# Optimization experiments

Hardware: AMD Instinct MI355X
Metric: run time of the kernel (lower is better)

Reference implementation:

```python
import jax, jax.numpy as jnp
import numpy as np

EPS = 1e-7
INF = 1e8
NUM_CLASSES = 80
SOFT_CENTER_RADIUS = 3.0
TOPK = 13
IOU_WEIGHT = 3.0

B, N, G, C = 16, 8400, 100, NUM_CLASSES
IMG = 640.0


def setup_inputs() -> dict:
    key = jax.random.key(0)
    ks = jax.random.split(key, 8)
    # anchor priors: centers in image, stride column (cx, cy, s, s)
    ctr = jax.random.uniform(ks[0], (N, 2)) * IMG
    stride = jnp.full((N, 1), 8.0)
    priors = jnp.concatenate([ctr, stride, stride], axis=-1)
    # predicted boxes: xyxy around random centers
    pc = jax.random.uniform(ks[1], (B, N, 2)) * IMG
    pwh = jax.random.uniform(ks[2], (B, N, 2)) * 64.0 + 8.0
    pred_bboxes = jnp.concatenate([pc - pwh / 2, pc + pwh / 2], axis=-1)
    pred_scores = jax.random.normal(ks[3], (B, N, C))
    # gt boxes: xyxy
    gc = jax.random.uniform(ks[4], (B, G, 2)) * (IMG - 40.0) + 20.0
    gwh = jax.random.uniform(ks[5], (B, G, 2)) * 128.0 + 16.0
    gt_bboxes = jnp.concatenate([gc - gwh / 2, gc + gwh / 2], axis=-1)
    gt_labels = jax.random.randint(ks[6], (B, G, 1), 0, NUM_CLASSES, dtype=jnp.int32)
    pad_bbox_flag = jnp.ones((B, G, 1), dtype=jnp.float32)
    gt_bboxes_area = gwh[..., 0] * gwh[..., 1]
    area_rule = jnp.array([0.0, 32.0, 96.0, 1.0e4], dtype=jnp.float32)
    return {
        'pred_bboxes': pred_bboxes, 'pred_scores': pred_scores, 'priors': priors,
        'gt_labels': gt_labels, 'gt_bboxes': gt_bboxes, 'pad_bbox_flag': pad_bbox_flag,
        'gt_bboxes_area': gt_bboxes_area, 'area_rule': area_rule,
    }


def _giou(b1, b2):
    # b1, b2 broadcastable [..., 4] xyxy -> GIoU [...]
    lt = jnp.maximum(b1[..., :2], b2[..., :2])
    rb = jnp.minimum(b1[..., 2:], b2[..., 2:])
    wh = jnp.clip(rb - lt, 0.0)
    overlap = wh[..., 0] * wh[..., 1]
    a1 = (b1[..., 2] - b1[..., 0]) * (b1[..., 3] - b1[..., 1])
    a2 = (b2[..., 2] - b2[..., 0]) * (b2[..., 3] - b2[..., 1])
    union = jnp.maximum(a1 + a2 - overlap, EPS)
    iou = overlap / union
    elt = jnp.minimum(b1[..., :2], b2[..., :2])
    erb = jnp.maximum(b1[..., 2:], b2[..., 2:])
    ewh = jnp.clip(erb - elt, 0.0)
    enclose = jnp.maximum(ewh[..., 0] * ewh[..., 1], EPS)
    return iou - (enclose - union) / enclose


def _forward(pred_bboxes, pred_scores, priors, gt_labels, gt_bboxes, pad_bbox_flag,
             gt_bboxes_area, area_rule):
    b, n, _ = pred_bboxes.shape
    g = gt_bboxes.shape[1]
    pts = priors[:, :2]                      # (N,2)
    # point-in-box test -> (B,N,G)
    lt = pts[None, :, None, :] - gt_bboxes[:, None, :, :2]
    rb = gt_bboxes[:, None, :, 2:] - pts[None, :, None, :]
    deltas = jnp.concatenate([lt, rb], axis=-1)          # (B,N,G,4)
    is_in = (jnp.min(deltas, axis=-1) > 0).astype(pred_bboxes.dtype)
    is_in = is_in * pad_bbox_flag[:, None, :, 0]
    # soft center prior
    gt_ctr = (gt_bboxes[..., :2] + gt_bboxes[..., 2:]) / 2.0
    strides = priors[:, 2]
    dist = jnp.sqrt(((pts[None, :, None, :] - gt_ctr[:, None, :, :]) ** 2).sum(-1))
    dist = dist / strides[None, :, None] * is_in
    soft_center_prior = jnp.power(10.0, dist - SOFT_CENTER_RADIUS) * is_in
    # pairwise GIoU (B,N,G)
    giou = _giou(pred_bboxes[:, :, None, :], gt_bboxes[:, None, :, :])
    pairwise_ious = jnp.abs(giou * is_in)
    iou_cost = -jnp.log(pairwise_ious + EPS) * IOU_WEIGHT
    # per-gt-class logit gather: (B,N,G)
    labels = gt_labels[..., 0].astype(jnp.int32)         # (B,G)
    idx = jnp.broadcast_to(labels[:, None, :], (b, n, g))
    logits = jnp.take_along_axis(pred_scores, idx, axis=2)
    sig = jax.nn.sigmoid(logits)
    scale = pairwise_ious - sig
    # stable BCE-with-logits against soft target pairwise_ious
    bce = jnp.maximum(logits, 0.0) - logits * pairwise_ious + jnp.log1p(jnp.exp(-jnp.abs(logits)))
    cls_cost = bce * jnp.exp(jnp.abs(scale) - 1.0) * jnp.abs(scale)
    cost = cls_cost + iou_cost + soft_center_prior
    in_mask = is_in > 0
    cost = jnp.where(in_mask, cost, INF)
    # dynamic-k matching
    k = min(TOPK, n)
    topk_ious = jax.lax.top_k(jnp.transpose(pairwise_ious, (0, 2, 1)), k)[0]  # (B,G,k)
    dyn_k = jnp.clip(topk_ious.sum(-1).astype(jnp.int32), 1, None)            # (B,G)
    ranks = jnp.argsort(jnp.argsort(cost, axis=1), axis=1)                    # (B,N,G)
    valid_gt = pad_bbox_flag[..., 0] > 0                                      # (B,G)
    matching = (ranks < dyn_k[:, None, :]) & valid_gt[:, None, :]             # (B,N,G)
    # resolve anchors matched to >1 gt: keep min-cost gt
    multi = matching.sum(-1) > 1                                              # (B,N)
    onehot_min = jax.nn.one_hot(jnp.argmin(cost, axis=-1), g, dtype=jnp.bool_)
    matching = jnp.where(multi[..., None], onehot_min, matching)
    fg_mask = matching.sum(-1) > 0                                            # (B,N)
    mf = matching.astype(pairwise_ious.dtype)
    matched_ious = (mf * pairwise_ious).sum(-1)                               # (B,N)
    matched_gt = jnp.argmax(mf, axis=-1)                                      # (B,N)
    # dense assignments
    assigned_labels = jnp.where(fg_mask, jnp.take_along_axis(labels, matched_gt, axis=1), NUM_CLASSES)
    gidx = jnp.broadcast_to(matched_gt[..., None], (b, n, 4))
    assigned_bboxes = jnp.where(fg_mask[..., None], jnp.take_along_axis(gt_bboxes, gidx, axis=1), 0.0)
    assign_metrics = jnp.where(fg_mask, matched_ious, 0.0)
    onehot = jax.nn.one_hot(assigned_labels, NUM_CLASSES + 1, dtype=pred_scores.dtype)[..., :NUM_CLASSES]
    assigned_scores = onehot * jnp.where(fg_mask, matched_ious, 1.0)[..., None]
    # per-class positive counts and dynamic class weights
    assigned_labels_num = (onehot * fg_mask[..., None].astype(onehot.dtype)).sum((0, 1))
    maxc = assigned_labels_num.max()
    dynamic_gt_class_weight = jnp.where(assigned_labels_num > 0,
                                        maxc / jnp.maximum(assigned_labels_num, 1.0), 1.0)
    assigned_labels_weights = jnp.where(fg_mask[..., None],
                                        dynamic_gt_class_weight[None, None, :],
                                        jnp.ones((), pred_scores.dtype))
    # gt area distribution (len(area_rule)-1, B, G)
    r2 = area_rule ** 2
    ga = gt_bboxes_area[None]
    area_dist = (ga >= r2[:-1, None, None]) & (ga < r2[1:, None, None]) & valid_gt[None]
    return (assigned_labels.astype(jnp.int32), assigned_labels_weights, assigned_bboxes,
            assigned_scores, assign_metrics, fg_mask, assigned_labels_num,
            dynamic_gt_class_weight, area_dist)


def reference(pred_bboxes, pred_scores, priors, gt_labels, gt_bboxes, pad_bbox_flag,
              gt_bboxes_area, area_rule):
    return _forward(pred_bboxes, pred_scores, priors, gt_labels, gt_bboxes,
                    pad_bbox_flag, gt_bboxes_area, area_rule)
```

## Files before the change

### kernel.cpp

```cpp
#include <hip/hip_runtime.h>

typedef unsigned long long u64;

#define BB 16
#define NN 8400
#define GG 100
#define CC 80
#define KTOP 13
#define EPSF 1e-7f
#define INFC 1e8f
#define MAXIN 1024
#define MAXMULTI (BB * GG * KTOP / 2)

static constexpr size_t kO_LAB  = 0;
static constexpr size_t kO_W    = (size_t)BB * NN;
static constexpr size_t kO_BB   = kO_W + (size_t)BB * NN * CC;
static constexpr size_t kO_SC   = kO_BB + (size_t)BB * NN * 4;
static constexpr size_t kO_MET  = kO_SC + (size_t)BB * NN * CC;
static constexpr size_t kO_FG   = kO_MET + (size_t)BB * NN;
static constexpr size_t kO_NUM  = kO_FG + (size_t)BB * NN;
static constexpr size_t kO_DYNW = kO_NUM + CC;
static constexpr size_t kO_AREA = kO_DYNW + CC;

__device__ __forceinline__ unsigned f2u(float x) {
    unsigned b = __float_as_uint(x);
    return (b & 0x80000000u) ? ~b : (b | 0x80000000u);
}
__device__ __forceinline__ float u2f(unsigned e) {
    return __uint_as_float((e & 0x80000000u) ? (e & 0x7fffffffu) : ~e);
}

__device__ __forceinline__ void pair_cost_iou_inside(
    float px, float py, float st,
    float p0, float p1, float p2, float p3,
    float g0, float g1, float g2, float g3,
    float lg, float flag,
    float& cost, float& piou)
{
    float gcx = (g0 + g2) * 0.5f, gcy = (g1 + g3) * 0.5f;
    float dx = px - gcx, dy = py - gcy;
    float dist = sqrtf(dx * dx + dy * dy) / st * flag;
    float scp = exp2f((dist - 3.0f) * 3.32192809488736f) * flag;
    float ix1 = fmaxf(p0, g0), iy1 = fmaxf(p1, g1);
    float ix2 = fminf(p2, g2), iy2 = fminf(p3, g3);
    float ow = fmaxf(ix2 - ix1, 0.0f), oh = fmaxf(iy2 - iy1, 0.0f);
    float ov = ow * oh;
    float a1 = (p2 - p0) * (p3 - p1);
    float a2 = (g2 - g0) * (g3 - g1);
    float uni = fmaxf(a1 + a2 - ov, EPSF);
    float iou = ov / uni;
    float ex1 = fminf(p0, g0), ey1 = fminf(p1, g1);
    float ex2 = fmaxf(p2, g2), ey2 = fmaxf(p3, g3);
    float ew = fmaxf(ex2 - ex1, 0.0f), eh = fmaxf(ey2 - ey1, 0.0f);
    float enc = fmaxf(ew * eh, EPSF);
    float giou = iou - (enc - uni) / enc;
    piou = fabsf(giou * flag);
    float iou_cost = -__logf(piou + EPSF) * 3.0f;
    float sig = 1.0f / (1.0f + __expf(-lg));
    float sc = piou - sig;
    float asc = fabsf(sc);
    float bce = fmaxf(lg, 0.0f) - lg * piou + log1pf(__expf(-fabsf(lg)));
    float cls = bce * __expf(asc - 1.0f) * asc;
    cost = cls + iou_cost + scp;
}

__device__ __forceinline__ void pair_cost_iou(
    float px, float py, float st,
    float p0, float p1, float p2, float p3,
    float g0, float g1, float g2, float g3,
    float lg, float flag,
    float& cost, float& piou)
{
    float l = px - g0, t = py - g1, r = g2 - px, d = g3 - py;
    float mn = fminf(fminf(l, t), fminf(r, d));
    float is_in = (mn > 0.0f) ? flag : 0.0f;
    float gcx = (g0 + g2) * 0.5f, gcy = (g1 + g3) * 0.5f;
    float dx = px - gcx, dy = py - gcy;
    float dist = sqrtf(dx * dx + dy * dy) / st * is_in;
    float scp = exp2f((dist - 3.0f) * 3.32192809488736f) * is_in;
    float ix1 = fmaxf(p0, g0), iy1 = fmaxf(p1, g1);
    float ix2 = fminf(p2, g2), iy2 = fminf(p3, g3);
    float ow = fmaxf(ix2 - ix1, 0.0f), oh = fmaxf(iy2 - iy1, 0.0f);
    float ov = ow * oh;
    float a1 = (p2 - p0) * (p3 - p1);
    float a2 = (g2 - g0) * (g3 - g1);
    float uni = fmaxf(a1 + a2 - ov, EPSF);
    float iou = ov / uni;
    float ex1 = fminf(p0, g0), ey1 = fminf(p1, g1);
    float ex2 = fmaxf(p2, g2), ey2 = fmaxf(p3, g3);
    float ew = fmaxf(ex2 - ex1, 0.0f), eh = fmaxf(ey2 - ey1, 0.0f);
    float enc = fmaxf(ew * eh, EPSF);
    float giou = iou - (enc - uni) / enc;
    piou = fabsf(giou * is_in);
    float iou_cost = -__logf(piou + EPSF) * 3.0f;
    float sig = 1.0f / (1.0f + __expf(-lg));
    float sc = piou - sig;
    float asc = fabsf(sc);
    float bce = fmaxf(lg, 0.0f) - lg * piou + log1pf(__expf(-fabsf(lg)));
    float cls = bce * __expf(asc - 1.0f) * asc;
    float cc = cls + iou_cost + scp;
    cost = (is_in > 0.0f) ? cc : INFC;
}

__device__ __forceinline__ u64 block_max_u64(u64 v, u64* s_red, int tid) {
    #pragma unroll
    for (int off = 32; off > 0; off >>= 1) {
        u64 o = __shfl_down(v, off, 64);
        if (o > v) v = o;
    }
    __syncthreads();
    if ((tid & 63) == 0) s_red[tid >> 6] = v;
    __syncthreads();
    u64 m = s_red[0];
    #pragma unroll
    for (int i = 1; i < 4; ++i) if (s_red[i] > m) m = s_red[i];
    return m;
}
__device__ __forceinline__ u64 block_min_u64(u64 v, u64* s_red, int tid) {
    #pragma unroll
    for (int off = 32; off > 0; off >>= 1) {
        u64 o = __shfl_down(v, off, 64);
        if (o < v) v = o;
    }
    __syncthreads();
    if ((tid & 63) == 0) s_red[tid >> 6] = v;
    __syncthreads();
    u64 m = s_red[0];
    #pragma unroll
    for (int i = 1; i < 4; ++i) if (s_red[i] < m) m = s_red[i];
    return m;
}

__global__ __launch_bounds__(256) void k1_match(
    const float* __restrict__ pred_bboxes,
    const float* __restrict__ pred_scores,
    const float* __restrict__ priors,
    const int*   __restrict__ gt_labels,
    const float* __restrict__ gt_bboxes,
    const float* __restrict__ pad_flag,
    int*   __restrict__ match_count,
    int*   __restrict__ match_g,
    float* __restrict__ match_iou)
{
    __shared__ int s_cnt;
    __shared__ int s_list[MAXIN];
    __shared__ u64 s_red[4];

    int bg = blockIdx.x;
    int b = bg / GG, g = bg - b * GG;
    int tid = threadIdx.x;

    float flag = pad_flag[bg];
    if (flag == 0.0f) return;

    if (tid == 0) s_cnt = 0;
    __syncthreads();

    float4 gb = *reinterpret_cast<const float4*>(gt_bboxes + (size_t)bg * 4);

    for (int n = tid; n < NN; n += 256) {
        float2 p = *reinterpret_cast<const float2*>(priors + (size_t)n * 4);
        float l = p.x - gb.x, t = p.y - gb.y;
        float r = gb.z - p.x, d = gb.w - p.y;
        float mn = fminf(fminf(l, t), fminf(r, d));
        if (mn > 0.0f) {
            int po = atomicAdd(&s_cnt, 1);
            if (po < MAXIN) s_list[po] = n;
        }
    }
    __syncthreads();
    int M = min(s_cnt, MAXIN);

    if (M == 0) {
        if (tid == 0) {
            int idx = b * NN;
            atomicAdd(&match_count[idx], 1);
            match_g[idx]   = g;
            match_iou[idx] = 0.0f;
        }
        return;
    }

    int lab = gt_labels[bg];

    u64 zs = ((u64)0x80000000u << 32) | (0x10000u + (unsigned)tid * 4u);
    u64 iK0 = zs, iK1 = zs + 1, iK2 = zs + 2, iK3 = zs + 3;
    u64 cK0 = ~0ull, cK1 = ~0ull, cK2 = ~0ull, cK3 = ~0ull;
    float cP0 = 0.f, cP1 = 0.f, cP2 = 0.f, cP3 = 0.f;

    for (int m = tid; m < M; m += 256) {
        int n = s_list[m];
        float4 pr = *reinterpret_cast<const float4*>(priors + (size_t)n * 4);
        float4 pb = *reinterpret_cast<const float4*>(pred_bboxes + ((size_t)b * NN + n) * 4);
        float lg = pred_scores[((size_t)b * NN + n) * CC + lab];
        float cost, piou;
        pair_cost_iou_inside(pr.x, pr.y, pr.z, pb.x, pb.y, pb.z, pb.w,
                             gb.x, gb.y, gb.z, gb.w, lg, flag, cost, piou);
        u64 ki = ((u64)f2u(piou) << 32) | (unsigned)n;
        if (ki > iK3) {
            iK3 = ki;
            if (iK3 > iK2) { u64 t0 = iK2; iK2 = iK3; iK3 = t0; }
            if (iK2 > iK1) { u64 t0 = iK1; iK1 = iK2; iK2 = t0; }
            if (iK1 > iK0) { u64 t0 = iK0; iK0 = iK1; iK1 = t0; }
        }
        u64 kc = ((u64)f2u(cost) << 32) | (unsigned)n;
        if (kc < cK3) {
            cK3 = kc; cP3 = piou;
            if (cK3 < cK2) { u64 t0 = cK2; cK2 = cK3; cK3 = t0; float f0 = cP2; cP2 = cP3; cP3 = f0; }
            if (cK2 < cK1) { u64 t0 = cK1; cK1 = cK2; cK2 = t0; float f0 = cP1; cP1 = cP2; cP2 = f0; }
            if (cK1 < cK0) { u64 t0 = cK0; cK0 = cK1; cK1 = t0; float f0 = cP0; cP0 = cP1; cP1 = f0; }
        }
    }

    float ksum = 0.0f;
    for (int it = 0; it < KTOP; ++it) {
        u64 mx = block_max_u64(iK0, s_red, tid);
        ksum += u2f((unsigned)(mx >> 32));
        if (iK0 == mx) { iK0 = iK1; iK1 = iK2; iK2 = iK3; iK3 = 0ull; }
    }
    int dyn_k = (int)ksum;
    if (dyn_k < 1) dyn_k = 1;

    for (int it = 0; it < dyn_k; ++it) {
        u64 mn = block_min_u64(cK0, s_red, tid);
        if (cK0 == mn) {
            int bi = (int)(mn & 0xffffffffu);
            int idx = b * NN + bi;
            atomicAdd(&match_count[idx], 1);
            match_g[idx]   = g;
            match_iou[idx] = cP0;
            cK0 = cK1; cP0 = cP1; cK1 = cK2; cP1 = cP2; cK2 = cK3; cP2 = cP3;
            cK3 = ~0ull;
        }
    }
}

__global__ __launch_bounds__(256) void k2a_resolve(
    const int*   __restrict__ gt_labels,
    const float* __restrict__ gt_bboxes,
    const int*   __restrict__ match_count,
    const int*   __restrict__ match_g,
    const float* __restrict__ match_iou,
    int*   __restrict__ r_lab,
    float* __restrict__ r_miou,
    int*   __restrict__ class_num,
    int*   __restrict__ multi_count,
    int*   __restrict__ multi_list,
    float* __restrict__ out)
{
    int i = blockIdx.x * 256 + threadIdx.x;
    if (i >= BB * NN) return;
    int cnt = match_count[i];
    if (cnt > 1) {
        int p = atomicAdd(multi_count, 1);
        multi_list[p] = i;
        return;
    }
    int b = i / NN;
    int lab = CC;
    float miou = 0.0f;
    float4 bb = make_float4(0.0f, 0.0f, 0.0f, 0.0f);
    if (cnt == 1) {
        int g = match_g[i];
        miou = match_iou[i];
        lab = gt_labels[b * GG + g];
        bb = *reinterpret_cast<const float4*>(gt_bboxes + (size_t)(b * GG + g) * 4);
        atomicAdd(&class_num[lab], 1);
    }
    r_lab[i]  = lab;
    r_miou[i] = miou;
    out[kO_LAB + i] = (float)lab;
    out[kO_FG  + i] = (cnt == 1) ? 1.0f : 0.0f;
    out[kO_MET + i] = miou;
    *reinterpret_cast<float4*>(out + kO_BB + (size_t)i * 4) = bb;
}

__global__ __launch_bounds__(256) void k2b_multi(
    const float* __restrict__ pred_bboxes,
    const float* __restrict__ pred_scores,
    const float* __restrict__ priors,
    const int*   __restrict__ gt_labels,
    const float* __restrict__ gt_bboxes,
    const float* __restrict__ pad_flag,
    const int*   __restrict__ multi_count,
    const int*   __restrict__ multi_list,
    int*   __restrict__ r_lab,
    float* __restrict__ r_miou,
    int*   __restrict__ class_num,
    float* __restrict__ out)
{
    int wid  = (blockIdx.x * 256 + threadIdx.x) >> 6;
    int lane = threadIdx.x & 63;
    int cnt = *multi_count;
    if (wid >= cnt) return;
    int i = multi_list[wid];
    int b = i / NN, n = i - b * NN;

    float4 pr = *reinterpret_cast<const float4*>(priors + (size_t)n * 4);
    float4 pb = *reinterpret_cast<const float4*>(pred_bboxes + (size_t)i * 4);

    u64 bestk = ~0ull;
    float bestiou = 0.0f;
    #pragma unroll
    for (int s = 0; s < 2; ++s) {
        int g = lane + s * 64;
        if (g < GG) {
            float flag = pad_flag[b * GG + g];
            float4 gb = *reinterpret_cast<const float4*>(gt_bboxes + (size_t)(b * GG + g) * 4);
            int lb = gt_labels[b * GG + g];
            float lg = pred_scores[(size_t)i * CC + lb];
            float cost, piou;
            pair_cost_iou(pr.x, pr.y, pr.z, pb.x, pb.y, pb.z, pb.w,
                          gb.x, gb.y, gb.z, gb.w, lg, flag, cost, piou);
            u64 k = ((u64)f2u(cost) << 32) | (unsigned)g;
            if (k < bestk) { bestk = k; bestiou = piou; }
        }
    }
    #pragma unroll
    for (int off = 32; off > 0; off >>= 1) {
        u64 ok = __shfl_down(bestk, off, 64);
        float op = __shfl_down(bestiou, off, 64);
        if (ok < bestk) { bestk = ok; bestiou = op; }
    }
    if (lane == 0) {
        int g = (int)(bestk & 0xffffffffu);
        int lab = gt_labels[b * GG + g];
        float4 bb = *reinterpret_cast<const float4*>(gt_bboxes + (size_t)(b * GG + g) * 4);
        atomicAdd(&class_num[lab], 1);
        r_lab[i]  = lab;
        r_miou[i] = bestiou;
        out[kO_LAB + i] = (float)lab;
        out[kO_FG  + i] = 1.0f;
        out[kO_MET + i] = bestiou;
        *reinterpret_cast<float4*>(out + kO_BB + (size_t)i * 4) = bb;
    }
}

__global__ void k3_weights(const int* __restrict__ class_num,
                           float* __restrict__ dynw,
                           float* __restrict__ out)
{
    int lane = threadIdx.x;
    int n0 = class_num[lane];
    int n1 = (lane < CC - 64) ? class_num[lane + 64] : 0;
    int m = max(n0, n1);
    #pragma unroll
    for (int off = 32; off > 0; off >>= 1) m = max(m, __shfl_down(m, off, 64));
    m = __shfl(m, 0, 64);
    float fm = (float)m;
    {
        float w = (n0 > 0) ? fm / fmaxf((float)n0, 1.0f) : 1.0f;
        dynw[lane] = w;
        out[kO_NUM  + lane] = (float)n0;
        out[kO_DYNW + lane] = w;
    }
    if (lane < CC - 64) {
        float w = (n1 > 0) ? fm / fmaxf((float)n1, 1.0f) : 1.0f;
        dynw[lane + 64] = w;
        out[kO_NUM  + lane + 64] = (float)n1;
        out[kO_DYNW + lane + 64] = w;
    }
}

__global__ __launch_bounds__(256) void k4_fill(
    const int*   __restrict__ r_lab,
    const float* __restrict__ r_miou,
    const float* __restrict__ dynw,
    float* __restrict__ out)
{
    __shared__ float s_w[CC];
    if (threadIdx.x < CC) s_w[threadIdx.x] = dynw[threadIdx.x];
    __syncthreads();
    unsigned t = blockIdx.x * 256u + threadIdx.x;
    unsigned i = t / 20u;
    unsigned cq = (t - i * 20u) * 4u;
    int lab = r_lab[i];
    float miou = r_miou[i];
    bool fg = lab < CC;
    unsigned ulab = (unsigned)lab;
    float4 sc, wv;
    sc.x = (ulab == cq + 0u) ? miou : 0.0f;
    sc.y = (ulab == cq + 1u) ? miou : 0.0f;
    sc.z = (ulab == cq + 2u) ? miou : 0.0f;
    sc.w = (ulab == cq + 3u) ? miou : 0.0f;
    wv.x = fg ? s_w[cq + 0u] : 1.0f;
    wv.y = fg ? s_w[cq + 1u] : 1.0f;
    wv.z = fg ? s_w[cq + 2u] : 1.0f;
    wv.w = fg ? s_w[cq + 3u] : 1.0f;
    size_t base = (size_t)i * CC + cq;
    *reinterpret_cast<float4*>(out + kO_SC + base) = sc;
    *reinterpret_cast<float4*>(out + kO_W  + base) = wv;
}

__global__ void k5_area(const float* __restrict__ gt_area,
                        const float* __restrict__ area_rule,
                        const float* __restrict__ pad_flag,
                        float* __restrict__ out)
{
    int idx = blockIdx.x * 256 + threadIdx.x;
    if (idx >= 3 * BB * GG) return;
    int z = idx / (BB * GG);
    int rem = idx - z * (BB * GG);
    float ga = gt_area[rem];
    float lo = area_rule[z] * area_rule[z];
    float hi = area_rule[z + 1] * area_rule[z + 1];
    bool v = (ga >= lo) && (ga < hi) && (pad_flag[rem] > 0.0f);
    out[kO_AREA + idx] = v ? 1.0f : 0.0f;
}

extern "C" void kernel_launch(void* const* d_in, const int* in_sizes, int n_in,
                              void* d_out, int out_size, void* d_ws, size_t ws_size,
                              hipStream_t stream)
{
    const float* pred_bboxes = (const float*)d_in[0];
    const float* pred_scores = (const float*)d_in[1];
    const float* priors      = (const float*)d_in[2];
    const int*   gt_labels   = (const int*)d_in[3];
    const float* gt_bboxes   = (const float*)d_in[4];
    const float* pad_flag    = (const float*)d_in[5];
    const float* gt_area     = (const float*)d_in[6];
    const float* area_rule   = (const float*)d_in[7];
    float* out = (float*)d_out;

    char* w = (char*)d_ws;
    int*   match_count = (int*)w;   w += (size_t)BB * NN * 4;
    int*   class_num   = (int*)w;   w += (size_t)CC * 4;
    int*   multi_count = (int*)w;   w += 4;
    int*   multi_list  = (int*)w;   w += (size_t)MAXMULTI * 4;
    int*   match_g     = (int*)w;   w += (size_t)BB * NN * 4;
    float* match_iou   = (float*)w; w += (size_t)BB * NN * 4;
    int*   r_lab       = (int*)w;   w += (size_t)BB * NN * 4;
    float* r_miou      = (float*)w; w += (size_t)BB * NN * 4;
    float* dynw        = (float*)w; w += (size_t)CC * 4;

    hipMemsetAsync(d_ws, 0, (size_t)(BB * NN + CC + 1) * 4, stream);

    k1_match<<<BB * GG, 256, 0, stream>>>(
        pred_bboxes, pred_scores, priors, gt_labels, gt_bboxes, pad_flag,
        match_count, match_g, match_iou);

    k2a_resolve<<<(BB * NN + 255) / 256, 256, 0, stream>>>(
        gt_labels, gt_bboxes, match_count, match_g, match_iou,
        r_lab, r_miou, class_num, multi_count, multi_list, out);

    k2b_multi<<<(MAXMULTI * 64 + 255) / 256, 256, 0, stream>>>(
        pred_bboxes, pred_scores, priors, gt_labels, gt_bboxes, pad_flag,
        multi_count, multi_list, r_lab, r_miou, class_num, out);

    k3_weights<<<1, 64, 0, stream>>>(class_num, dynw, out);

    k4_fill<<<(int)(((size_t)BB * NN * (CC / 4) + 255) / 256), 256, 0, stream>>>(
        r_lab, r_miou, dynw, out);

    k5_area<<<(3 * BB * GG + 255) / 256, 256, 0, stream>>>(
        gt_area, area_rule, pad_flag, out);
}
```

Baseline: 240.1 us.

## Replace block-wide top-k reductions with per-wave selection and merge kernels

The top-k IoU and dynamic-k cost selections in the match kernel now run per wave with xor shuffles, and a single wave merges the candidates. This replaces a block reduction with two barriers per iteration. The separate multi-match resolve kernel is folded into the resolve kernel through a ballot loop, the weights and area kernels are merged, and the prior scan is unrolled. The result is fewer launches and barriers, at the cost of divergent per-wave loops inside the resolve kernel.

```diff
diff --git a/kernel.cpp b/kernel.cpp
--- a/kernel.cpp
+++ b/kernel.cpp
@@ -10,7 +10,6 @@
 #define EPSF 1e-7f
 #define INFC 1e8f
 #define MAXIN 1024
-#define MAXMULTI (BB * GG * KTOP / 2)
 
 static constexpr size_t kO_LAB  = 0;
 static constexpr size_t kO_W    = (size_t)BB * NN;
@@ -102,35 +101,6 @@
     cost = (is_in > 0.0f) ? cc : INFC;
 }
 
-__device__ __forceinline__ u64 block_max_u64(u64 v, u64* s_red, int tid) {
-    #pragma unroll
-    for (int off = 32; off > 0; off >>= 1) {
-        u64 o = __shfl_down(v, off, 64);
-        if (o > v) v = o;
-    }
-    __syncthreads();
-    if ((tid & 63) == 0) s_red[tid >> 6] = v;
-    __syncthreads();
-    u64 m = s_red[0];
-    #pragma unroll
-    for (int i = 1; i < 4; ++i) if (s_red[i] > m) m = s_red[i];
-    return m;
-}
-__device__ __forceinline__ u64 block_min_u64(u64 v, u64* s_red, int tid) {
-    #pragma unroll
-    for (int off = 32; off > 0; off >>= 1) {
-        u64 o = __shfl_down(v, off, 64);
-        if (o < v) v = o;
-    }
-    __syncthreads();
-    if ((tid & 63) == 0) s_red[tid >> 6] = v;
-    __syncthreads();
-    u64 m = s_red[0];
-    #pragma unroll
-    for (int i = 1; i < 4; ++i) if (s_red[i] < m) m = s_red[i];
-    return m;
-}
-
 __global__ __launch_bounds__(256) void k1_match(
     const float* __restrict__ pred_bboxes,
     const float* __restrict__ pred_scores,
@@ -142,13 +112,17 @@
     int*   __restrict__ match_g,
     float* __restrict__ match_iou)
 {
-    __shared__ int s_cnt;
-    __shared__ int s_list[MAXIN];
-    __shared__ u64 s_red[4];
+    __shared__ int   s_cnt;
+    __shared__ int   s_list[MAXIN];
+    __shared__ u64   s_cand[4 * KTOP];
+    __shared__ float s_candP[4 * KTOP];
+    __shared__ int   s_dynk;
 
     int bg = blockIdx.x;
     int b = bg / GG, g = bg - b * GG;
-    int tid = threadIdx.x;
+    int tid  = threadIdx.x;
+    int lane = tid & 63;
+    int w    = tid >> 6;
 
     float flag = pad_flag[bg];
     if (flag == 0.0f) return;
@@ -158,11 +132,22 @@
 
     float4 gb = *reinterpret_cast<const float4*>(gt_bboxes + (size_t)bg * 4);
 
-    for (int n = tid; n < NN; n += 256) {
-        float2 p = *reinterpret_cast<const float2*>(priors + (size_t)n * 4);
-        float l = p.x - gb.x, t = p.y - gb.y;
-        float r = gb.z - p.x, d = gb.w - p.y;
-        float mn = fminf(fminf(l, t), fminf(r, d));
+    #pragma unroll 4
+    for (int k = 0; k < 32; ++k) {
+        int n = tid + (k << 8);
+        float4 p = *reinterpret_cast<const float4*>(priors + (size_t)n * 4);
+        float mn = fminf(fminf(p.x - gb.x, p.y - gb.y),
+                         fminf(gb.z - p.x, gb.w - p.y));
+        if (mn > 0.0f) {
+            int po = atomicAdd(&s_cnt, 1);
+            if (po < MAXIN) s_list[po] = n;
+        }
+    }
+    if (tid < NN - 8192) {
+        int n = tid + 8192;
+        float4 p = *reinterpret_cast<const float4*>(priors + (size_t)n * 4);
+        float mn = fminf(fminf(p.x - gb.x, p.y - gb.y),
+                         fminf(gb.z - p.x, gb.w - p.y));
         if (mn > 0.0f) {
             int po = atomicAdd(&s_cnt, 1);
             if (po < MAXIN) s_list[po] = n;
@@ -212,153 +197,202 @@
         }
     }
 
-    float ksum = 0.0f;
-    for (int it = 0; it < KTOP; ++it) {
-        u64 mx = block_max_u64(iK0, s_red, tid);
-        ksum += u2f((unsigned)(mx >> 32));
-        if (iK0 == mx) { iK0 = iK1; iK1 = iK2; iK2 = iK3; iK3 = 0ull; }
-    }
-    int dyn_k = (int)ksum;
-    if (dyn_k < 1) dyn_k = 1;
-
-    for (int it = 0; it < dyn_k; ++it) {
-        u64 mn = block_min_u64(cK0, s_red, tid);
-        if (cK0 == mn) {
-            int bi = (int)(mn & 0xffffffffu);
-            int idx = b * NN + bi;
-            atomicAdd(&match_count[idx], 1);
-            match_g[idx]   = g;
-            match_iou[idx] = cP0;
+    for (int r = 0; r < KTOP; ++r) {
+        u64 h = iK0;
+        #pragma unroll
+        for (int off = 1; off < 64; off <<= 1) {
+            u64 o = __shfl_xor(h, off, 64);
+            if (o > h) h = o;
+        }
+        if (lane == 0) s_cand[w * KTOP + r] = h;
+        if (iK0 == h) { iK0 = iK1; iK1 = iK2; iK2 = iK3; iK3 = 0ull; }
+    }
+    __syncthreads();
+    if (w == 0) {
+        u64 kk = (lane < 4 * KTOP) ? s_cand[lane] : 0ull;
+        float ks = 0.0f;
+        for (int r = 0; r < KTOP; ++r) {
+            u64 h = kk;
+            #pragma unroll
+            for (int off = 1; off < 64; off <<= 1) {
+                u64 o = __shfl_xor(h, off, 64);
+                if (o > h) h = o;
+            }
+            ks += u2f((unsigned)(h >> 32));
+            if (kk == h) kk = 0ull;
+        }
+        if (lane == 0) { int dk = (int)ks; s_dynk = (dk < 1) ? 1 : dk; }
+    }
+    __syncthreads();
+    int dyn_k = s_dynk;
+
+    for (int r = 0; r < dyn_k; ++r) {
+        u64 h = cK0;
+        #pragma unroll
+        for (int off = 1; off < 64; off <<= 1) {
+            u64 o = __shfl_xor(h, off, 64);
+            if (o < h) h = o;
+        }
+        if (cK0 == h) {
+            s_cand[w * KTOP + r]  = h;
+            s_candP[w * KTOP + r] = cP0;
             cK0 = cK1; cP0 = cP1; cK1 = cK2; cP1 = cP2; cK2 = cK3; cP2 = cP3;
             cK3 = ~0ull;
         }
     }
-}
-
-__global__ __launch_bounds__(256) void k2a_resolve(
+    __syncthreads();
+    if (w == 0) {
+        int tot = 4 * dyn_k;
+        u64 kk = ~0ull; float pp = 0.0f;
+        if (lane < tot) {
+            int wv = lane / dyn_k;
+            int r  = lane - wv * dyn_k;
+            kk = s_cand[wv * KTOP + r];
+            pp = s_candP[wv * KTOP + r];
+        }
+        for (int r = 0; r < dyn_k; ++r) {
+            u64 h = kk;
+            #pragma unroll
+            for (int off = 1; off < 64; off <<= 1) {
+                u64 o = __shfl_xor(h, off, 64);
+                if (o < h) h = o;
+            }
+            if (kk == h && h != ~0ull) {
+                int bi = (int)(h & 0xffffffffu);
+                int idx = b * NN + bi;
+                atomicAdd(&match_count[idx], 1);
+                match_g[idx]   = g;
+                match_iou[idx] = pp;
+                kk = ~0ull;
+            }
+        }
+    }
+}
+
+__global__ __launch_bounds__(256) void k2_resolve(
+    const float* __restrict__ pred_bboxes,
+    const float* __restrict__ pred_scores,
+    const float* __restrict__ priors,
     const int*   __restrict__ gt_labels,
     const float* __restrict__ gt_bboxes,
+    const float* __restrict__ pad_flag,
     const int*   __restrict__ match_count,
     const int*   __restrict__ match_g,
     const float* __restrict__ match_iou,
     int*   __restrict__ r_lab,
     float* __restrict__ r_miou,
     int*   __restrict__ class_num,
-    int*   __restrict__ multi_count,
-    int*   __restrict__ multi_list,
     float* __restrict__ out)
 {
     int i = blockIdx.x * 256 + threadIdx.x;
-    if (i >= BB * NN) return;
+    int lane = threadIdx.x & 63;
     int cnt = match_count[i];
-    if (cnt > 1) {
-        int p = atomicAdd(multi_count, 1);
-        multi_list[p] = i;
-        return;
-    }
     int b = i / NN;
+
     int lab = CC;
     float miou = 0.0f;
-    float4 bb = make_float4(0.0f, 0.0f, 0.0f, 0.0f);
+    float4 bbx = make_float4(0.0f, 0.0f, 0.0f, 0.0f);
+
     if (cnt == 1) {
         int g = match_g[i];
+        int gi = b * GG + g;
         miou = match_iou[i];
-        lab = gt_labels[b * GG + g];
-        bb = *reinterpret_cast<const float4*>(gt_bboxes + (size_t)(b * GG + g) * 4);
-        atomicAdd(&class_num[lab], 1);
-    }
+        lab = gt_labels[gi];
+        bbx = *reinterpret_cast<const float4*>(gt_bboxes + (size_t)gi * 4);
+    }
+
+    u64 mask = __ballot(cnt > 1);
+    while (mask) {
+        int src = __builtin_ctzll(mask);
+        mask &= mask - 1;
+        int ii = (i & ~63) | src;
+        int b2 = ii / NN, n2 = ii - b2 * NN;
+        float4 pr = *reinterpret_cast<const float4*>(priors + (size_t)n2 * 4);
+        float4 pb = *reinterpret_cast<const float4*>(pred_bboxes + (size_t)ii * 4);
+        u64 bk = ~0ull; float bp = 0.0f;
+        #pragma unroll
+        for (int s = 0; s < 2; ++s) {
+            int gg = lane + (s << 6);
+            if (gg < GG) {
+                int gi = b2 * GG + gg;
+                float fl = pad_flag[gi];
+                float4 gbx = *reinterpret_cast<const float4*>(gt_bboxes + (size_t)gi * 4);
+                int lb = gt_labels[gi];
+                float lg = pred_scores[(size_t)ii * CC + lb];
+                float cost, piou;
+                pair_cost_iou(pr.x, pr.y, pr.z, pb.x, pb.y, pb.z, pb.w,
+                              gbx.x, gbx.y, gbx.z, gbx.w, lg, fl, cost, piou);
+                u64 k = ((u64)f2u(cost) << 32) | (unsigned)gg;
+                if (k < bk) { bk = k; bp = piou; }
+            }
+        }
+        #pragma unroll
+        for (int off = 1; off < 64; off <<= 1) {
+            u64 ok = __shfl_xor(bk, off, 64);
+            float op = __shfl_xor(bp, off, 64);
+            if (ok < bk) { bk = ok; bp = op; }
+        }
+        if (lane == src) {
+            int gw = (int)(bk & 0xffffffffu);
+            int gi = b2 * GG + gw;
+            lab = gt_labels[gi];
+            miou = bp;
+            bbx = *reinterpret_cast<const float4*>(gt_bboxes + (size_t)gi * 4);
+        }
+    }
+
+    bool fg = cnt > 0;
+    if (fg) atomicAdd(&class_num[lab], 1);
     r_lab[i]  = lab;
     r_miou[i] = miou;
     out[kO_LAB + i] = (float)lab;
-    out[kO_FG  + i] = (cnt == 1) ? 1.0f : 0.0f;
+    out[kO_FG  + i] = fg ? 1.0f : 0.0f;
     out[kO_MET + i] = miou;
-    *reinterpret_cast<float4*>(out + kO_BB + (size_t)i * 4) = bb;
-}
-
-__global__ __launch_bounds__(256) void k2b_multi(
-    const float* __restrict__ pred_bboxes,
-    const float* __restrict__ pred_scores,
-    const float* __restrict__ priors,
-    const int*   __restrict__ gt_labels,
-    const float* __restrict__ gt_bboxes,
+    *reinterpret_cast<float4*>(out + kO_BB + (size_t)i * 4) = bbx;
+}
+
+__global__ __launch_bounds__(256) void k35_weights_area(
+    const int*   __restrict__ class_num,
+    float* __restrict__ dynw,
+    const float* __restrict__ gt_area,
+    const float* __restrict__ area_rule,
     const float* __restrict__ pad_flag,
-    const int*   __restrict__ multi_count,
-    const int*   __restrict__ multi_list,
-    int*   __restrict__ r_lab,
-    float* __restrict__ r_miou,
-    int*   __restrict__ class_num,
     float* __restrict__ out)
 {
-    int wid  = (blockIdx.x * 256 + threadIdx.x) >> 6;
-    int lane = threadIdx.x & 63;
-    int cnt = *multi_count;
-    if (wid >= cnt) return;
-    int i = multi_list[wid];
-    int b = i / NN, n = i - b * NN;
-
-    float4 pr = *reinterpret_cast<const float4*>(priors + (size_t)n * 4);
-    float4 pb = *reinterpret_cast<const float4*>(pred_bboxes + (size_t)i * 4);
-
-    u64 bestk = ~0ull;
-    float bestiou = 0.0f;
-    #pragma unroll
-    for (int s = 0; s < 2; ++s) {
-        int g = lane + s * 64;
-        if (g < GG) {
-            float flag = pad_flag[b * GG + g];
-            float4 gb = *reinterpret_cast<const float4*>(gt_bboxes + (size_t)(b * GG + g) * 4);
-            int lb = gt_labels[b * GG + g];
-            float lg = pred_scores[(size_t)i * CC + lb];
-            float cost, piou;
-            pair_cost_iou(pr.x, pr.y, pr.z, pb.x, pb.y, pb.z, pb.w,
-                          gb.x, gb.y, gb.z, gb.w, lg, flag, cost, piou);
-            u64 k = ((u64)f2u(cost) << 32) | (unsigned)g;
-            if (k < bestk) { bestk = k; bestiou = piou; }
-        }
-    }
-    #pragma unroll
-    for (int off = 32; off > 0; off >>= 1) {
-        u64 ok = __shfl_down(bestk, off, 64);
-        float op = __shfl_down(bestiou, off, 64);
-        if (ok < bestk) { bestk = ok; bestiou = op; }
-    }
-    if (lane == 0) {
-        int g = (int)(bestk & 0xffffffffu);
-        int lab = gt_labels[b * GG + g];
-        float4 bb = *reinterpret_cast<const float4*>(gt_bboxes + (size_t)(b * GG + g) * 4);
-        atomicAdd(&class_num[lab], 1);
-        r_lab[i]  = lab;
-        r_miou[i] = bestiou;
-        out[kO_LAB + i] = (float)lab;
-        out[kO_FG  + i] = 1.0f;
-        out[kO_MET + i] = bestiou;
-        *reinterpret_cast<float4*>(out + kO_BB + (size_t)i * 4) = bb;
-    }
-}
-
-__global__ void k3_weights(const int* __restrict__ class_num,
-                           float* __restrict__ dynw,
-                           float* __restrict__ out)
-{
-    int lane = threadIdx.x;
-    int n0 = class_num[lane];
-    int n1 = (lane < CC - 64) ? class_num[lane + 64] : 0;
-    int m = max(n0, n1);
-    #pragma unroll
-    for (int off = 32; off > 0; off >>= 1) m = max(m, __shfl_down(m, off, 64));
-    m = __shfl(m, 0, 64);
-    float fm = (float)m;
-    {
-        float w = (n0 > 0) ? fm / fmaxf((float)n0, 1.0f) : 1.0f;
-        dynw[lane] = w;
-        out[kO_NUM  + lane] = (float)n0;
-        out[kO_DYNW + lane] = w;
-    }
-    if (lane < CC - 64) {
-        float w = (n1 > 0) ? fm / fmaxf((float)n1, 1.0f) : 1.0f;
-        dynw[lane + 64] = w;
-        out[kO_NUM  + lane + 64] = (float)n1;
-        out[kO_DYNW + lane + 64] = w;
+    if (blockIdx.x == 0) {
+        int lane = threadIdx.x;
+        if (lane < 64) {
+            int n0 = class_num[lane];
+            int n1 = (lane < CC - 64) ? class_num[lane + 64] : 0;
+            int m = max(n0, n1);
+            #pragma unroll
+            for (int off = 32; off > 0; off >>= 1) m = max(m, __shfl_down(m, off, 64));
+            m = __shfl(m, 0, 64);
+            float fm = (float)m;
+            {
+                float wv = (n0 > 0) ? fm / fmaxf((float)n0, 1.0f) : 1.0f;
+                dynw[lane] = wv;
+                out[kO_NUM  + lane] = (float)n0;
+                out[kO_DYNW + lane] = wv;
+            }
+            if (lane < CC - 64) {
+                float wv = (n1 > 0) ? fm / fmaxf((float)n1, 1.0f) : 1.0f;
+                dynw[lane + 64] = wv;
+                out[kO_NUM  + lane + 64] = (float)n1;
+                out[kO_DYNW + lane + 64] = wv;
+            }
+        }
+    } else {
+        int idx = (blockIdx.x - 1) * 256 + threadIdx.x;
+        if (idx < 3 * BB * GG) {
+            int z = idx / (BB * GG);
+            int rem = idx - z * (BB * GG);
+            float ga = gt_area[rem];
+            float lo = area_rule[z] * area_rule[z];
+            float hi = area_rule[z + 1] * area_rule[z + 1];
+            bool v = (ga >= lo) && (ga < hi) && (pad_flag[rem] > 0.0f);
+            out[kO_AREA + idx] = v ? 1.0f : 0.0f;
+        }
     }
 }
 
@@ -392,22 +426,6 @@
     *reinterpret_cast<float4*>(out + kO_W  + base) = wv;
 }
 
-__global__ void k5_area(const float* __restrict__ gt_area,
-                        const float* __restrict__ area_rule,
-                        const float* __restrict__ pad_flag,
-                        float* __restrict__ out)
-{
-    int idx = blockIdx.x * 256 + threadIdx.x;
-    if (idx >= 3 * BB * GG) return;
-    int z = idx / (BB * GG);
-    int rem = idx - z * (BB * GG);
-    float ga = gt_area[rem];
-    float lo = area_rule[z] * area_rule[z];
-    float hi = area_rule[z + 1] * area_rule[z + 1];
-    bool v = (ga >= lo) && (ga < hi) && (pad_flag[rem] > 0.0f);
-    out[kO_AREA + idx] = v ? 1.0f : 0.0f;
-}
-
 extern "C" void kernel_launch(void* const* d_in, const int* in_sizes, int n_in,
                               void* d_out, int out_size, void* d_ws, size_t ws_size,
                               hipStream_t stream)
@@ -425,33 +443,25 @@
     char* w = (char*)d_ws;
     int*   match_count = (int*)w;   w += (size_t)BB * NN * 4;
     int*   class_num   = (int*)w;   w += (size_t)CC * 4;
-    int*   multi_count = (int*)w;   w += 4;
-    int*   multi_list  = (int*)w;   w += (size_t)MAXMULTI * 4;
     int*   match_g     = (int*)w;   w += (size_t)BB * NN * 4;
     float* match_iou   = (float*)w; w += (size_t)BB * NN * 4;
     int*   r_lab       = (int*)w;   w += (size_t)BB * NN * 4;
     float* r_miou      = (float*)w; w += (size_t)BB * NN * 4;
     float* dynw        = (float*)w; w += (size_t)CC * 4;
 
-    hipMemsetAsync(d_ws, 0, (size_t)(BB * NN + CC + 1) * 4, stream);
+    hipMemsetAsync(d_ws, 0, (size_t)(BB * NN + CC) * 4, stream);
 
     k1_match<<<BB * GG, 256, 0, stream>>>(
         pred_bboxes, pred_scores, priors, gt_labels, gt_bboxes, pad_flag,
         match_count, match_g, match_iou);
 
-    k2a_resolve<<<(BB * NN + 255) / 256, 256, 0, stream>>>(
-        gt_labels, gt_bboxes, match_count, match_g, match_iou,
-        r_lab, r_miou, class_num, multi_count, multi_list, out);
-
-    k2b_multi<<<(MAXMULTI * 64 + 255) / 256, 256, 0, stream>>>(
+    k2_resolve<<<BB * NN / 256, 256, 0, stream>>>(
         pred_bboxes, pred_scores, priors, gt_labels, gt_bboxes, pad_flag,
-        multi_count, multi_list, r_lab, r_miou, class_num, out);
-
-    k3_weights<<<1, 64, 0, stream>>>(class_num, dynw, out);
-
-    k4_fill<<<(int)(((size_t)BB * NN * (CC / 4) + 255) / 256), 256, 0, stream>>>(
+        match_count, match_g, match_iou, r_lab, r_miou, class_num, out);
+
+    k35_weights_area<<<1 + (3 * BB * GG + 255) / 256, 256, 0, stream>>>(
+        class_num, dynw, gt_area, area_rule, pad_flag, out);
+
+    k4_fill<<<(int)((size_t)BB * NN * (CC / 4) / 256), 256, 0, stream>>>(
         r_lab, r_miou, dynw, out);
-
-    k5_area<<<(3 * BB * GG + 255) / 256, 256, 0, stream>>>(
-        gt_area, area_rule, pad_flag, out);
-}
+}
```

After: 232.2 us. 1.03x faster.
